# Kernel tuning notes

Measured on AMD Instinct MI355X. Metric: run time of the kernel, lower is better.

The kernel has to match this reference:

```python
import jax, jax.numpy as jnp
import numpy as np

LOSS_WEIGHT = 1.0  # init kwarg
B = 16   # number of segments
S = 2048 # points per segment (uniform; offsets are cumulative multiples of S)


def setup_inputs() -> dict:
    key = jax.random.key(0)
    k1, k2, k3, k4 = jax.random.split(key, 4)
    coord = jax.random.normal(k1, (B * S, 3), dtype=jnp.float32)
    coord_transformed = jax.random.normal(k2, (B * S, 3), dtype=jnp.float32)
    R = jax.random.normal(k3, (B, 3, 3), dtype=jnp.float32)
    t = jax.random.normal(k4, (B, 3), dtype=jnp.float32)
    offset = (jnp.arange(B, dtype=jnp.int64) + 1) * S          # cumulative end offsets
    offset_trans = (jnp.arange(B, dtype=jnp.int64) + 1) * S
    return {"coord": coord, "coord_transformed": coord_transformed,
            "R": R, "t": t, "offset": offset, "offset_trans": offset_trans}


def reference(coord, coord_transformed, R, t, offset, offset_trans):
    # Uniform segments: reshape ragged-by-offset layout to [B, S, 3].
    b = R.shape[0]
    s = coord.shape[0] // b
    src = coord.reshape(b, s, 3)
    tgt = coord_transformed.reshape(b, -1, 3)
    # Per-segment rigid transform: (Ri @ src.T).T + ti
    src_t = jnp.einsum('bij,bnj->bni', R, src) + t[:, None, :]
    # Squared pairwise distances [B, S, S] (min of dist then square == min of sq-dist).
    d2 = (jnp.sum(src_t * src_t, axis=-1)[:, :, None]
          + jnp.sum(tgt * tgt, axis=-1)[:, None, :]
          - 2.0 * jnp.einsum('bnd,bmd->bnm', src_t, tgt))
    nn_d2 = jnp.min(jnp.maximum(d2, 0.0), axis=2)  # [B, S] NN squared distance
    per_seg = jnp.mean(nn_d2, axis=1)              # reduction='mean' within segment
    loss = jnp.mean(per_seg)                       # reduction='mean' over segments
    return loss * LOSS_WEIGHT
```

## Files before the change

### kernel.cpp

```cpp
#include <hip/hip_runtime.h>
#include <math.h>


#define THREADS 512
#define SRC_BLK 128
#define PART_STRIDE 18

typedef __attribute__((ext_vector_type(8))) _Float16 half8;
typedef __attribute__((ext_vector_type(16))) float f32x16;

__device__ __forceinline__ unsigned short f16b(float x) {
    _Float16 hv = (_Float16)x;
    return __builtin_bit_cast(unsigned short, hv);
}
__device__ __forceinline__ float f16tof(unsigned short u) {
    return (float)__builtin_bit_cast(_Float16, u);
}

__global__ __launch_bounds__(THREADS)
void nn_mfma_kernel(const float* __restrict__ coord,
                    const float* __restrict__ coord_t,
                    const float* __restrict__ Rm,
                    const float* __restrict__ tv,
                    float* __restrict__ ws,
                    int S, int NSC) {
    __shared__ uint4 Bfrag[2048];
    __shared__ float part[128 * PART_STRIDE];
    __shared__ float SN_lds[128];
    __shared__ float wsum[2];

    const int tid  = threadIdx.x;
    const int bid  = blockIdx.x;
    const int b    = bid / NSC;
    const int sc   = bid - b * NSC;
    const int w    = tid >> 6;
    const int lane = tid & 63;
    const int col  = lane & 31;
    const int kh   = lane >> 5;
    const int wsrc = w >> 1;
    const int h    = w & 1;

    if (tid * 4 < S) {
        const float* tb = coord_t + (size_t)b * S * 3;
        const float4* g4 = reinterpret_cast<const float4*>(tb) + (size_t)tid * 3;
        const float4 q0 = g4[0], q1 = g4[1], q2 = g4[2];
        const float px[4] = {q0.x, q0.w, q1.z, q2.y};
        const float py[4] = {q0.y, q1.x, q1.w, q2.z};
        const float pz[4] = {q0.z, q1.y, q2.x, q2.w};
        #pragma unroll
        for (int k = 0; k < 4; ++k) {
            const float tx = px[k], ty = py[k], tz = pz[k];
            const float TN = __builtin_fmaf(tz, tz, __builtin_fmaf(ty, ty, tx*tx));
            const unsigned uhx = f16b(-2.f*tx), uhy = f16b(-2.f*ty), uhz = f16b(-2.f*tz);
            const unsigned TNh = f16b(TN);
            const unsigned TNl = f16b(TN - f16tof((unsigned short)TNh));
            uint4 wv;
            wv.x = uhx | (uhy << 16);
            wv.y = uhz | (uhx << 16);
            wv.z = uhy | (uhz << 16);
            wv.w = TNh | (TNl << 16);
            Bfrag[tid * 4 + k] = wv;
        }
    }

    half8 afrag;
    #pragma unroll
    for (int i = 0; i < 8; ++i) afrag[i] = (_Float16)0.0f;
    {
        const float* Rb = Rm + (size_t)b * 9;
        const float r00=Rb[0], r01=Rb[1], r02=Rb[2];
        const float r10=Rb[3], r11=Rb[4], r12=Rb[5];
        const float r20=Rb[6], r21=Rb[7], r22=Rb[8];
        const float t0=tv[3*b], t1=tv[3*b+1], t2=tv[3*b+2];

        const float* sp = coord + ((size_t)b*S + (size_t)sc*SRC_BLK + wsrc*32 + col) * 3;
        const float x = sp[0], y = sp[1], z = sp[2];
        const float sx = __builtin_fmaf(r00,x,__builtin_fmaf(r01,y,__builtin_fmaf(r02,z,t0)));
        const float sy = __builtin_fmaf(r10,x,__builtin_fmaf(r11,y,__builtin_fmaf(r12,z,t1)));
        const float sz = __builtin_fmaf(r20,x,__builtin_fmaf(r21,y,__builtin_fmaf(r22,z,t2)));
        const float SN = __builtin_fmaf(sz, sz, __builtin_fmaf(sy, sy, sx*sx));
        if (h == 0 && kh == 0) SN_lds[wsrc*32 + col] = SN;
        if (kh == 0) {
            const _Float16 shx = (_Float16)sx, shy = (_Float16)sy, shz = (_Float16)sz;
            afrag[0] = shx; afrag[1] = shy; afrag[2] = shz;
            afrag[3] = (_Float16)(sx - (float)shx);
            afrag[4] = (_Float16)(sy - (float)shy);
            afrag[5] = (_Float16)(sz - (float)shz);
            afrag[6] = (_Float16)1.0f; afrag[7] = (_Float16)1.0f;
        }
    }

    __syncthreads();

    f32x16 zf, mn;
    #pragma unroll
    for (int r = 0; r < 16; ++r) { zf[r] = 0.0f; mn[r] = 1e30f; }

    const uint4* Bp = &Bfrag[h*1024 + col];
    if (S == 2048) {
        #pragma unroll 4
        for (int it = 0; it < 16; ++it) {
            const half8 b0 = *reinterpret_cast<const half8*>(Bp + it*64);
            const half8 b1 = *reinterpret_cast<const half8*>(Bp + it*64 + 32);
            const f32x16 aA = __builtin_amdgcn_mfma_f32_32x32x16_f16(afrag, b0, zf, 0, 0, 0);
            const f32x16 aB = __builtin_amdgcn_mfma_f32_32x32x16_f16(afrag, b1, zf, 0, 0, 0);
            #pragma unroll
            for (int r = 0; r < 16; ++r)
                mn[r] = fminf(fminf(mn[r], aA[r]), aB[r]);
        }
    } else {
        const int nit = S >> 7;
        for (int it = 0; it < nit; ++it) {
            const half8 b0 = *reinterpret_cast<const half8*>(Bp + it*64);
            const half8 b1 = *reinterpret_cast<const half8*>(Bp + it*64 + 32);
            const f32x16 aA = __builtin_amdgcn_mfma_f32_32x32x16_f16(afrag, b0, zf, 0, 0, 0);
            const f32x16 aB = __builtin_amdgcn_mfma_f32_32x32x16_f16(afrag, b1, zf, 0, 0, 0);
            #pragma unroll
            for (int r = 0; r < 16; ++r)
                mn[r] = fminf(fminf(mn[r], aA[r]), aB[r]);
        }
    }

    #pragma unroll
    for (int r = 0; r < 16; ++r) {
        float v = mn[r];
        v = fminf(v, __shfl_xor(v, 1, 64));
        v = fminf(v, __shfl_xor(v, 2, 64));
        if ((col & 3) == 0) {
            const int row = (r & 3) + 8*(r >> 2) + 4*kh;
            part[(wsrc*32 + row)*PART_STRIDE + h*8 + (col >> 2)] = v;
        }
    }
    __syncthreads();

    float acc = 0.0f;
    if (tid < 128) {
        const float* pp = &part[tid * PART_STRIDE];
        float m = pp[0];
        #pragma unroll
        for (int j = 1; j < 16; ++j) m = fminf(m, pp[j]);
        acc = fmaxf(SN_lds[tid] + m, 0.0f);
        #pragma unroll
        for (int off = 32; off > 0; off >>= 1) acc += __shfl_down(acc, off, 64);
        if ((tid & 63) == 0) wsum[tid >> 6] = acc;
    }
    __syncthreads();
    if (tid == 0) ws[bid] = wsum[0] + wsum[1];
}

__global__ __launch_bounds__(256)
void final_kernel(const float* __restrict__ partial, int n,
                  float* __restrict__ out, float scale) {
    float v = (threadIdx.x < n) ? partial[threadIdx.x] : 0.0f;
    #pragma unroll
    for (int off = 32; off > 0; off >>= 1) v += __shfl_down(v, off, 64);
    __shared__ float sm[4];
    if ((threadIdx.x & 63) == 0) sm[threadIdx.x >> 6] = v;
    __syncthreads();
    if (threadIdx.x == 0) out[0] = (sm[0] + sm[1] + sm[2] + sm[3]) * scale;
}

extern "C" void kernel_launch(void* const* d_in, const int* in_sizes, int n_in,
                              void* d_out, int out_size, void* d_ws, size_t ws_size,
                              hipStream_t stream) {
    const float* coord   = (const float*)d_in[0];
    const float* coord_t = (const float*)d_in[1];
    const float* Rm      = (const float*)d_in[2];
    const float* tv      = (const float*)d_in[3];

    const int B = in_sizes[2] / 9;
    const int S = in_sizes[0] / (3 * B);
    const int NSC = S / SRC_BLK;
    const int nblk = B * NSC;

    float* ws  = (float*)d_ws;
    float* out = (float*)d_out;

    nn_mfma_kernel<<<nblk, THREADS, 0, stream>>>(
        coord, coord_t, Rm, tv, ws, S, NSC);

    final_kernel<<<1, 256, 0, stream>>>(
        ws, nblk, out, 1.0f / ((float)B * (float)S));
}
```

Before: 13.13 us.

## Fuse final reduction into main kernel via atomic sum and last-block counter

Replaces the second reduction kernel launch with a global atomic add of per-block sums plus an atomic ticket counter, so the last finishing block writes the scaled loss and resets the accumulator. This removes one kernel launch and its dependency gap. It also generalizes target staging to a strided loop and drops the S==2048 specialized unrolled loop, which may lose unrolling benefits. The atomic float sum makes the result order-nondeterministic, and correctness relies on the workspace starting zeroed and the counter wrapping modulo nblk.

```diff
diff --git a/kernel.cpp b/kernel.cpp
--- a/kernel.cpp
+++ b/kernel.cpp
@@ -22,8 +22,10 @@
                     const float* __restrict__ coord_t,
                     const float* __restrict__ Rm,
                     const float* __restrict__ tv,
-                    float* __restrict__ ws,
-                    int S, int NSC) {
+                    float* __restrict__ sum_p,
+                    unsigned int* __restrict__ cnt_p,
+                    float* __restrict__ out,
+                    int S, int NSC, int nblk, float scale) {
     __shared__ uint4 Bfrag[2048];
     __shared__ float part[128 * PART_STRIDE];
     __shared__ float SN_lds[128];
@@ -40,26 +42,28 @@
     const int wsrc = w >> 1;
     const int h    = w & 1;
 
-    if (tid * 4 < S) {
+    {
         const float* tb = coord_t + (size_t)b * S * 3;
-        const float4* g4 = reinterpret_cast<const float4*>(tb) + (size_t)tid * 3;
-        const float4 q0 = g4[0], q1 = g4[1], q2 = g4[2];
-        const float px[4] = {q0.x, q0.w, q1.z, q2.y};
-        const float py[4] = {q0.y, q1.x, q1.w, q2.z};
-        const float pz[4] = {q0.z, q1.y, q2.x, q2.w};
-        #pragma unroll
-        for (int k = 0; k < 4; ++k) {
-            const float tx = px[k], ty = py[k], tz = pz[k];
-            const float TN = __builtin_fmaf(tz, tz, __builtin_fmaf(ty, ty, tx*tx));
-            const unsigned uhx = f16b(-2.f*tx), uhy = f16b(-2.f*ty), uhz = f16b(-2.f*tz);
-            const unsigned TNh = f16b(TN);
-            const unsigned TNl = f16b(TN - f16tof((unsigned short)TNh));
-            uint4 wv;
-            wv.x = uhx | (uhy << 16);
-            wv.y = uhz | (uhx << 16);
-            wv.z = uhy | (uhz << 16);
-            wv.w = TNh | (TNl << 16);
-            Bfrag[tid * 4 + k] = wv;
+        for (int g = tid; g * 4 < S; g += THREADS) {
+            const float4* g4 = reinterpret_cast<const float4*>(tb) + (size_t)g * 3;
+            const float4 q0 = g4[0], q1 = g4[1], q2 = g4[2];
+            const float px[4] = {q0.x, q0.w, q1.z, q2.y};
+            const float py[4] = {q0.y, q1.x, q1.w, q2.z};
+            const float pz[4] = {q0.z, q1.y, q2.x, q2.w};
+            #pragma unroll
+            for (int k = 0; k < 4; ++k) {
+                const float tx = px[k], ty = py[k], tz = pz[k];
+                const float TN = __builtin_fmaf(tz, tz, __builtin_fmaf(ty, ty, tx*tx));
+                const unsigned uhx = f16b(-2.f*tx), uhy = f16b(-2.f*ty), uhz = f16b(-2.f*tz);
+                const unsigned TNh = f16b(TN);
+                const unsigned TNl = f16b(TN - f16tof((unsigned short)TNh));
+                uint4 wv;
+                wv.x = uhx | (uhy << 16);
+                wv.y = uhz | (uhx << 16);
+                wv.z = uhy | (uhz << 16);
+                wv.w = TNh | (TNl << 16);
+                Bfrag[g * 4 + k] = wv;
+            }
         }
     }
 
@@ -97,28 +101,15 @@
     for (int r = 0; r < 16; ++r) { zf[r] = 0.0f; mn[r] = 1e30f; }
 
     const uint4* Bp = &Bfrag[h*1024 + col];
-    if (S == 2048) {
-        #pragma unroll 4
-        for (int it = 0; it < 16; ++it) {
-            const half8 b0 = *reinterpret_cast<const half8*>(Bp + it*64);
-            const half8 b1 = *reinterpret_cast<const half8*>(Bp + it*64 + 32);
-            const f32x16 aA = __builtin_amdgcn_mfma_f32_32x32x16_f16(afrag, b0, zf, 0, 0, 0);
-            const f32x16 aB = __builtin_amdgcn_mfma_f32_32x32x16_f16(afrag, b1, zf, 0, 0, 0);
-            #pragma unroll
-            for (int r = 0; r < 16; ++r)
-                mn[r] = fminf(fminf(mn[r], aA[r]), aB[r]);
-        }
-    } else {
-        const int nit = S >> 7;
-        for (int it = 0; it < nit; ++it) {
-            const half8 b0 = *reinterpret_cast<const half8*>(Bp + it*64);
-            const half8 b1 = *reinterpret_cast<const half8*>(Bp + it*64 + 32);
-            const f32x16 aA = __builtin_amdgcn_mfma_f32_32x32x16_f16(afrag, b0, zf, 0, 0, 0);
-            const f32x16 aB = __builtin_amdgcn_mfma_f32_32x32x16_f16(afrag, b1, zf, 0, 0, 0);
-            #pragma unroll
-            for (int r = 0; r < 16; ++r)
-                mn[r] = fminf(fminf(mn[r], aA[r]), aB[r]);
-        }
+    const int nit = S >> 7;
+    for (int it = 0; it < nit; ++it) {
+        const half8 b0 = *reinterpret_cast<const half8*>(Bp + it*64);
+        const half8 b1 = *reinterpret_cast<const half8*>(Bp + it*64 + 32);
+        const f32x16 aA = __builtin_amdgcn_mfma_f32_32x32x16_f16(afrag, b0, zf, 0, 0, 0);
+        const f32x16 aB = __builtin_amdgcn_mfma_f32_32x32x16_f16(afrag, b1, zf, 0, 0, 0);
+        #pragma unroll
+        for (int r = 0; r < 16; ++r)
+            mn[r] = fminf(fminf(mn[r], aA[r]), aB[r]);
     }
 
     #pragma unroll
@@ -145,19 +136,22 @@
         if ((tid & 63) == 0) wsum[tid >> 6] = acc;
     }
     __syncthreads();
-    if (tid == 0) ws[bid] = wsum[0] + wsum[1];
-}
 
-__global__ __launch_bounds__(256)
-void final_kernel(const float* __restrict__ partial, int n,
-                  float* __restrict__ out, float scale) {
-    float v = (threadIdx.x < n) ? partial[threadIdx.x] : 0.0f;
-    #pragma unroll
-    for (int off = 32; off > 0; off >>= 1) v += __shfl_down(v, off, 64);
-    __shared__ float sm[4];
-    if ((threadIdx.x & 63) == 0) sm[threadIdx.x >> 6] = v;
-    __syncthreads();
-    if (threadIdx.x == 0) out[0] = (sm[0] + sm[1] + sm[2] + sm[3]) * scale;
+    if (tid == 0) {
+        const float bsum = wsum[0] + wsum[1];
+        (void)__hip_atomic_fetch_add(sum_p, bsum, __ATOMIC_RELAXED,
+                                     __HIP_MEMORY_SCOPE_AGENT);
+        asm volatile("s_waitcnt vmcnt(0)" ::: "memory");
+        const unsigned t = __hip_atomic_fetch_add(cnt_p, 1u, __ATOMIC_RELAXED,
+                                                  __HIP_MEMORY_SCOPE_AGENT);
+        if ((t % (unsigned)nblk) == (unsigned)(nblk - 1)) {
+            const float total = __hip_atomic_fetch_add(sum_p, 0.0f,
+                                 __ATOMIC_RELAXED, __HIP_MEMORY_SCOPE_AGENT);
+            out[0] = total * scale;
+            __hip_atomic_store(sum_p, 0.0f, __ATOMIC_RELAXED,
+                               __HIP_MEMORY_SCOPE_AGENT);
+        }
+    }
 }
 
 extern "C" void kernel_launch(void* const* d_in, const int* in_sizes, int n_in,
@@ -173,12 +167,11 @@
     const int NSC = S / SRC_BLK;
     const int nblk = B * NSC;
 
-    float* ws  = (float*)d_ws;
+    float* sum_p = (float*)d_ws;
+    unsigned int* cnt_p = (unsigned int*)((char*)d_ws + 4);
     float* out = (float*)d_out;
 
     nn_mfma_kernel<<<nblk, THREADS, 0, stream>>>(
-        coord, coord_t, Rm, tv, ws, S, NSC);
-
-    final_kernel<<<1, 256, 0, stream>>>(
-        ws, nblk, out, 1.0f / ((float)B * (float)S));
+        coord, coord_t, Rm, tv, sum_p, cnt_p, out,
+        S, NSC, nblk, 1.0f / ((float)B * (float)S));
 }
```

Measured after the change: 17.12 us. 30.4% more time.
